# Kernel optimization log

Hardware: AMD Instinct MI355X
Metric: run time of the kernel (lower is better)

The kernel has to match this reference:

```python
import jax, jax.numpy as jnp
from jax import lax
import numpy as np

N_ATOMS, N_BONDS, N_GRAPHS = 8192, 32768, 256
EMBED, HIDDEN, DEPTH = 32, 256, 10
ATOM_VOCAB, BOND_VOCAB = 200, 10


def setup_inputs() -> dict:
    key = jax.random.key(0)
    ks = jax.random.split(key, 16)
    f = lambda k, *sh: jax.random.normal(k, sh, dtype=jnp.float32) * 0.05
    return {
        "atom_features": jax.random.randint(ks[0], (N_ATOMS,), 0, ATOM_VOCAB),
        "bond_features": jax.random.randint(ks[1], (N_BONDS,), 0, BOND_VOCAB),
        "adjacency_matrix": jax.random.randint(ks[2], (N_ATOMS, N_ATOMS), 0, 2, dtype=jnp.int32),
        "batch_indices": jax.random.randint(ks[3], (N_ATOMS,), 0, N_GRAPHS),
        "atom_emb": f(ks[4], ATOM_VOCAB, EMBED),
        "bond_emb": f(ks[5], BOND_VOCAB, EMBED),
        "msg_W": f(ks[6], DEPTH, HIDDEN, 2 * EMBED),
        "msg_b": f(ks[7], DEPTH, HIDDEN),
        "gru_Wih": f(ks[8], DEPTH, 3 * EMBED, HIDDEN),
        "gru_Whh": f(ks[9], DEPTH, 3 * EMBED, EMBED),
        "gru_bih": f(ks[10], DEPTH, 3 * EMBED),
        "gru_bhh": f(ks[11], DEPTH, 3 * EMBED),
        "pool_W": f(ks[12], HIDDEN, EMBED),
        "pool_b": f(ks[13], HIDDEN),
    }


def _gmpn(atom_emb, bond_emb, msg_W, msg_b, gru_Wih, gru_Whh, gru_bih, gru_bhh,
          pool_W, pool_b, atom_features, bond_features, adjacency_matrix, batch_indices):
    H = atom_emb[atom_features]                       # [N, E]
    A = (adjacency_matrix > 0).astype(H.dtype)        # [N, N] 0/1
    deg = A.sum(axis=1)                               # [N]
    has_nb = deg > 0
    inv_deg = jnp.where(has_nb, 1.0 / jnp.maximum(deg, 1.0), 0.0)[:, None]

    def layer(h, params):
        W, b, wih, whh, b_ih, b_hh = params
        # mean_j Linear([h_i ; h_j]) = W1 h_i + W2 mean_j h_j + b
        neigh_mean = (A @ h) * inv_deg                # [N, E]
        W1, W2 = W[:, :EMBED], W[:, EMBED:]
        msg = h @ W1.T + neigh_mean @ W2.T + b        # [N, HIDDEN]
        msg = jnp.where(has_nb[:, None], msg, 0.0)    # zero message if no neighbors
        # single-step GRU: input=msg, hidden state=h
        gi = msg @ wih.T + b_ih
        gh = h @ whh.T + b_hh
        ir, iz, inn = jnp.split(gi, 3, axis=-1)
        hr, hz, hn = jnp.split(gh, 3, axis=-1)
        r = jax.nn.sigmoid(ir + hr)
        z = jax.nn.sigmoid(iz + hz)
        n = jnp.tanh(inn + r * hn)
        h_new = (1.0 - z) * n + z * h                 # [N, E]
        return h_new, None

    H, _ = lax.scan(layer, H, (msg_W, msg_b, gru_Wih, gru_Whh, gru_bih, gru_bhh))

    # per-graph mean pooling (zeros for empty graphs), then global_pool linear
    seg_sum = jax.ops.segment_sum(H, batch_indices, num_segments=N_GRAPHS)
    cnt = jax.ops.segment_sum(jnp.ones((H.shape[0],), H.dtype), batch_indices, num_segments=N_GRAPHS)
    graph_mean = jnp.where(cnt[:, None] > 0, seg_sum / jnp.maximum(cnt, 1.0)[:, None], 0.0)
    graph_embeddings = graph_mean @ pool_W.T + pool_b  # [G, HIDDEN]

    bond_embeddings = bond_emb[bond_features]          # [B, E]
    return H, bond_embeddings, graph_embeddings


def reference(atom_features, bond_features, adjacency_matrix, batch_indices,
              atom_emb, bond_emb, msg_W, msg_b, gru_Wih, gru_Whh, gru_bih, gru_bhh,
              pool_W, pool_b):
    return _gmpn(atom_emb, bond_emb, msg_W, msg_b, gru_Wih, gru_Whh, gru_bih, gru_bhh,
                 pool_W, pool_b, atom_features, bond_features, adjacency_matrix, batch_indices)
```

## Files before the change

kernel.cpp:

```cpp
#include <hip/hip_runtime.h>
#include <stdint.h>

typedef __bf16 bf16x8 __attribute__((ext_vector_type(8)));
typedef float f32x4 __attribute__((ext_vector_type(4)));

__device__ __forceinline__ float b2f(unsigned short u){
  unsigned int t = ((unsigned int)u) << 16;
  return __builtin_bit_cast(float, t);
}
__device__ __forceinline__ unsigned short f2b(float f){
  unsigned int x = __builtin_bit_cast(unsigned int, f);
  x = x + 0x7FFFu + ((x >> 16) & 1u);
  return (unsigned short)(x >> 16);
}
__device__ __forceinline__ void spread8(unsigned int B, unsigned int w[4]){
  unsigned int m = __umul24(B, 0x8001u);
  w[0] = __umul24(m & 0x00010001u, 0x3F80u);
  w[1] = __umul24(m & 0x00040004u, 0x0FE0u);
  w[2] = __umul24(m & 0x00100010u, 0x03F8u);
  w[3] = __umul24(m & 0x00400040u, 0x00FEu);
}
__device__ __forceinline__ float fsig(float x){ return 1.f/(1.f + __expf(-x)); }
__device__ __forceinline__ float ftanh(float x){ return 1.f - 2.f/(__expf(2.f*x) + 1.f); }

__global__ void k_init(const int* __restrict__ adj, unsigned int* __restrict__ mask3,
                       int* __restrict__ deg,
                       const void* s_msgW, const void* s_msgb, const void* s_wih,
                       const void* s_whh, const void* s_bih, const void* s_bhh,
                       const void* s_poolW, const void* s_poolb,
                       const unsigned short* __restrict__ aemb_u16,
                       const int* __restrict__ bft, const void* __restrict__ braw,
                       unsigned short* __restrict__ cw,
                       float* __restrict__ seg, float* __restrict__ cnt,
                       int* __restrict__ flag,
                       unsigned short* __restrict__ outB16, float* __restrict__ outB32){
  int b = blockIdx.x, t = threadIdx.x;
  if (b < 8192){
    int tid = b*256 + t;
    int rb  = tid >> 12;
    int rem = tid & 4095;
    int kgg = rem >> 6;
    int L   = rem & 63;
    int lc = L & 15, q = L >> 4;
    int row = rb*16 + lc;
    const int* arow = adj + (size_t)row*8192 + kgg*128 + q*8;
    unsigned int dw = 0; int pc = 0;
    #pragma unroll
    for (int s=0;s<4;s++){
      const int* p = arow + s*32;
      unsigned int bb = 0;
      #pragma unroll
      for (int j=0;j<8;j++) bb |= (p[j] > 0 ? 1u : 0u) << j;
      dw |= bb << (8*s);
      pc += __popc(bb);
    }
    mask3[tid] = dw;
    pc += __shfl_xor(pc, 16);
    pc += __shfl_xor(pc, 32);
    if (q == 0) atomicAdd(deg + row, pc);
    return;
  }
  unsigned int uu = aemb_u16[2*t];
  int e = (int)((uu >> 7) & 0xFF);
  unsigned long long vote = __ballot(e >= 100 && e <= 127);
  int isb = (__popcll(vote) > 32) ? 1 : 0;
  if (b < 9963){
    int id = (b - 8192)*256 + t;
    if (id < 453248){
      const void* src; int off;
      if      (id < 163840){ src = s_msgW;  off = id; }
      else if (id < 166400){ src = s_msgb;  off = id - 163840; }
      else if (id < 412160){ src = s_wih;   off = id - 166400; }
      else if (id < 442880){ src = s_whh;   off = id - 412160; }
      else if (id < 443840){ src = s_bih;   off = id - 442880; }
      else if (id < 444800){ src = s_bhh;   off = id - 443840; }
      else if (id < 452992){ src = s_poolW; off = id - 444800; }
      else                 { src = s_poolb; off = id - 452992; }
      cw[id] = isb ? ((const unsigned short*)src)[off]
                   : f2b(((const float*)src)[off]);
    }
  } else if (b < 9996){
    int id2 = (b - 9963)*256 + t;
    if (id2 < 8192) seg[id2] = 0.f;
    if (id2 < 256) cnt[id2] = 0.f;
    if (b == 9963 && t == 0) flag[0] = isb;
  } else {
    int id = (b - 9996)*256 + t;
    int e2 = id >> 5, c = id & 31;
    int idx = bft[e2]*32 + c;
    if (isb) outB16[id] = ((const unsigned short*)braw)[idx];
    else     outB32[id] = ((const float*)braw)[idx];
  }
}

__global__ void k_zero(int* __restrict__ deg){
  deg[blockIdx.x*256 + threadIdx.x] = 0;
}

__global__ void k_embed(const int* __restrict__ af, const void* __restrict__ araw,
                        const int* __restrict__ flag,
                        float* __restrict__ hf32, uint4* __restrict__ hfrag){
  __shared__ __align__(16) float sh[512];
  int t = threadIdx.x;
  int r = t >> 5, c = t & 31;
  int row = blockIdx.x*16 + r;
  int idx = af[row]*32 + c;
  float f;
  if (flag[0]) f = b2f(((const unsigned short*)araw)[idx]);
  else         f = ((const float*)araw)[idx];
  hf32[row*32 + c] = f;
  sh[r*32 + c] = f;
  __syncthreads();
  if (t < 64){
    int nt = t >> 5, Lq = t & 31;
    int ks32 = blockIdx.x >> 1, half = blockIdx.x & 1;
    int col = nt*16 + (Lq & 15);
    int rbase = (Lq >> 4)*8;
    unsigned int w[4];
    #pragma unroll
    for (int p=0;p<4;p++){
      unsigned int lo = f2b(sh[(rbase + 2*p    )*32 + col]);
      unsigned int hi = f2b(sh[(rbase + 2*p + 1)*32 + col]);
      w[p] = lo | (hi << 16);
    }
    hfrag[(ks32*2 + nt)*64 + half*32 + Lq] = make_uint4(w[0],w[1],w[2],w[3]);
  }
}

__launch_bounds__(512, 1)
__global__ void k_layer(const unsigned int* __restrict__ mask3,
                        const uint4* __restrict__ hfragIn,
                        unsigned int* __restrict__ hfragOut,
                        float* __restrict__ hf32,
                        const int* __restrict__ deg,
                        const unsigned short* __restrict__ msgW,
                        const unsigned short* __restrict__ msgb,
                        const unsigned short* __restrict__ wih,
                        const unsigned short* __restrict__ whh,
                        const unsigned short* __restrict__ bih,
                        const unsigned short* __restrict__ bhh,
                        const int* __restrict__ bidx,
                        float* __restrict__ seg, float* __restrict__ cnt,
                        unsigned short* __restrict__ out16, float* __restrict__ out32,
                        const int* __restrict__ flag, int last)
{
  __shared__ __align__(16) float uni[8448];
  __shared__ __align__(16) unsigned short sA[32][72];
  __shared__ __align__(16) unsigned short smsg[32][264];
  __shared__ int sdeg[32];

  const int t = threadIdx.x, b = blockIdx.x;
  const int w = t >> 6, L = t & 63;
  const int q = L >> 4, lc = L & 15;
  const int r0 = t >> 4;
  const int cl = t & 15;
  const int r  = b*32 + r0;
  const int isb = flag[0];
  const int dgr = deg[r];
  const float invr = dgr > 0 ? 1.f/(float)dgr : 0.f;
  float h0 = hf32[r*32 + cl];
  float h1 = hf32[r*32 + 16 + cl];
  sA[r0][cl]    = f2b(h0);
  sA[r0][16+cl] = f2b(h1);
  if (cl == 0) sdeg[r0] = dgr;

  {
    f32x4 a00={0,0,0,0}, a01={0,0,0,0}, a10={0,0,0,0}, a11={0,0,0,0};
    const unsigned int* mp = mask3 + (size_t)b*8192 + w*512 + L;
    const uint4* bp = hfragIn + (size_t)w*4096 + L;
    unsigned int mw0 = mp[0];
    unsigned int mw1 = mp[4096];
    uint4 cb[8];
    #pragma unroll
    for (int s=0;s<4;s++){ cb[2*s] = bp[s*128]; cb[2*s+1] = bp[s*128 + 64]; }
    for (int g=0; g<8; g++){
      unsigned int nm0 = 0, nm1 = 0;
      uint4 nb[8];
      if (g < 7){
        nm0 = mp[(g+1)*64];
        nm1 = mp[4096 + (g+1)*64];
        #pragma unroll
        for (int s=0;s<4;s++){
          nb[2*s]   = bp[((g+1)*4 + s)*128];
          nb[2*s+1] = bp[((g+1)*4 + s)*128 + 64];
        }
      }
      #pragma unroll
      for (int s=0; s<4; s++){
        union { unsigned int u[4]; bf16x8 v; } A0, A1, B0, B1;
        spread8((mw0 >> (8*s)) & 0xFFu, A0.u);
        spread8((mw1 >> (8*s)) & 0xFFu, A1.u);
        uint4 u0 = cb[2*s], u1 = cb[2*s+1];
        B0.u[0]=u0.x; B0.u[1]=u0.y; B0.u[2]=u0.z; B0.u[3]=u0.w;
        B1.u[0]=u1.x; B1.u[1]=u1.y; B1.u[2]=u1.z; B1.u[3]=u1.w;
        a00 = __builtin_amdgcn_mfma_f32_16x16x32_bf16(A0.v, B0.v, a00, 0,0,0);
        a01 = __builtin_amdgcn_mfma_f32_16x16x32_bf16(A0.v, B1.v, a01, 0,0,0);
        a10 = __builtin_amdgcn_mfma_f32_16x16x32_bf16(A1.v, B0.v, a10, 0,0,0);
        a11 = __builtin_amdgcn_mfma_f32_16x16x32_bf16(A1.v, B1.v, a11, 0,0,0);
      }
      mw0 = nm0; mw1 = nm1;
      if (g < 7){
        #pragma unroll
        for (int u=0;u<8;u++) cb[u] = nb[u];
      }
    }
    float* sp = uni + w*1056;
    #pragma unroll
    for (int rg=0; rg<4; rg++){
      int rw = q*4 + rg;
      sp[rw*33 + lc]         = a00[rg];
      sp[rw*33 + 16 + lc]    = a01[rg];
      sp[(16+rw)*33 + lc]    = a10[rg];
      sp[(16+rw)*33 + 16+lc] = a11[rg];
    }
  }
  __syncthreads();
  {
    float s0 = 0.f, s1 = 0.f;
    #pragma unroll
    for (int ww=0; ww<8; ww++){
      s0 += uni[ww*1056 + r0*33 + cl];
      s1 += uni[ww*1056 + r0*33 + 16 + cl];
    }
    sA[r0][32+cl] = f2b(s0*invr);
    sA[r0][48+cl] = f2b(s1*invr);
  }
  __syncthreads();
  {
    int rt = w & 1, ntb = (w >> 1)*4;
    union { uint4 u; bf16x8 v; } A0, A1;
    A0.u = *(const uint4*)&sA[rt*16 + lc][q*8];
    A1.u = *(const uint4*)&sA[rt*16 + lc][32 + q*8];
    int sd[4];
    #pragma unroll
    for (int rg=0; rg<4; rg++) sd[rg] = sdeg[rt*16 + q*4 + rg];
    #pragma unroll
    for (int i=0; i<4; i++){
      int nt = ntb + i;
      union { uint4 u; bf16x8 v; } B0, B1;
      B0.u = *(const uint4*)(msgW + (size_t)(nt*16 + lc)*64 + q*8);
      B1.u = *(const uint4*)(msgW + (size_t)(nt*16 + lc)*64 + 32 + q*8);
      f32x4 am = {0,0,0,0};
      am = __builtin_amdgcn_mfma_f32_16x16x32_bf16(A0.v, B0.v, am, 0,0,0);
      am = __builtin_amdgcn_mfma_f32_16x16x32_bf16(A1.v, B1.v, am, 0,0,0);
      float bv = b2f(msgb[nt*16 + lc]);
      #pragma unroll
      for (int rg=0; rg<4; rg++){
        int rw = rt*16 + q*4 + rg;
        float v = am[rg] + bv;
        if (sd[rg] == 0) v = 0.f;
        smsg[rw][nt*16 + lc] = f2b(v);
      }
    }
  }
  __syncthreads();
  {
    float* sgi = uni;
    float* sgh = uni + 3200;
    if (w < 6){
      int nt = w;
      f32x4 g0 = {0,0,0,0}, g1 = {0,0,0,0};
      #pragma unroll
      for (int ks=0; ks<8; ks++){
        union { uint4 u; bf16x8 v; } A0, A1, B;
        B.u  = *(const uint4*)(wih + (size_t)(nt*16 + lc)*256 + ks*32 + q*8);
        A0.u = *(const uint4*)&smsg[lc][ks*32 + q*8];
        A1.u = *(const uint4*)&smsg[16 + lc][ks*32 + q*8];
        g0 = __builtin_amdgcn_mfma_f32_16x16x32_bf16(A0.v, B.v, g0, 0,0,0);
        g1 = __builtin_amdgcn_mfma_f32_16x16x32_bf16(A1.v, B.v, g1, 0,0,0);
      }
      #pragma unroll
      for (int rg=0; rg<4; rg++){
        sgi[(q*4+rg)*100    + nt*16 + lc] = g0[rg];
        sgi[(16+q*4+rg)*100 + nt*16 + lc] = g1[rg];
      }
    } else {
      int rt = w - 6;
      union { uint4 u; bf16x8 v; } A;
      A.u = *(const uint4*)&sA[rt*16 + lc][q*8];
      #pragma unroll
      for (int nt=0; nt<6; nt++){
        union { uint4 u; bf16x8 v; } B;
        B.u = *(const uint4*)(whh + (size_t)(nt*16 + lc)*32 + q*8);
        f32x4 hh = {0,0,0,0};
        hh = __builtin_amdgcn_mfma_f32_16x16x32_bf16(A.v, B.v, hh, 0,0,0);
        #pragma unroll
        for (int rg=0; rg<4; rg++)
          sgh[(rt*16 + q*4+rg)*100 + nt*16 + lc] = hh[rg];
      }
    }
  }
  __syncthreads();
  {
    const float* sgi = uni;
    const float* sgh = uni + 3200;
    float ir0 = sgi[r0*100 + cl]    + b2f(bih[cl]),    hr0 = sgh[r0*100 + cl]    + b2f(bhh[cl]);
    float iz0 = sgi[r0*100 + 32+cl] + b2f(bih[32+cl]), hz0 = sgh[r0*100 + 32+cl] + b2f(bhh[32+cl]);
    float in0 = sgi[r0*100 + 64+cl] + b2f(bih[64+cl]), hn0 = sgh[r0*100 + 64+cl] + b2f(bhh[64+cl]);
    float ir1 = sgi[r0*100 + 16+cl] + b2f(bih[16+cl]), hr1 = sgh[r0*100 + 16+cl] + b2f(bhh[16+cl]);
    float iz1 = sgi[r0*100 + 48+cl] + b2f(bih[48+cl]), hz1 = sgh[r0*100 + 48+cl] + b2f(bhh[48+cl]);
    float in1 = sgi[r0*100 + 80+cl] + b2f(bih[80+cl]), hn1 = sgh[r0*100 + 80+cl] + b2f(bhh[80+cl]);
    float rr0 = fsig(ir0 + hr0), zz0 = fsig(iz0 + hz0);
    float rr1 = fsig(ir1 + hr1), zz1 = fsig(iz1 + hz1);
    float nn0 = ftanh(in0 + rr0*hn0);
    float nn1 = ftanh(in1 + rr1*hn1);
    h0 = (1.f - zz0)*nn0 + zz0*h0;
    h1 = (1.f - zz1)*nn1 + zz1*h1;
    hf32[r*32 + cl]      = h0;
    hf32[r*32 + 16 + cl] = h1;
    unsigned int m0 = f2b(h0), m1 = f2b(h1);
    unsigned int p0 = (unsigned int)__shfl_xor((int)m0, 16);
    unsigned int p1 = (unsigned int)__shfl_xor((int)m1, 16);
    if ((r & 1) == 0){
      int ks32 = r >> 5, Lf = ((r >> 3) & 3)*16 + cl, pidx = (r & 7) >> 1;
      hfragOut[((ks32*2 + 0)*64 + Lf)*4 + pidx] = m0 | (p0 << 16);
      hfragOut[((ks32*2 + 1)*64 + Lf)*4 + pidx] = m1 | (p1 << 16);
    }
    if (last){
      if (isb){ out16[r*32 + cl] = (unsigned short)m0; out16[r*32 + 16 + cl] = (unsigned short)m1; }
      else    { out32[r*32 + cl] = h0; out32[r*32 + 16 + cl] = h1; }
      int gb = bidx[r];
      atomicAdd(seg + gb*32 + cl, h0);
      atomicAdd(seg + gb*32 + 16 + cl, h1);
      if (cl == 0) atomicAdd(cnt + gb, 1.f);
    }
  }
}

__global__ void k_pool(const float* __restrict__ seg, const float* __restrict__ cnt,
                       const unsigned short* __restrict__ pw, const unsigned short* __restrict__ pb,
                       const int* __restrict__ flag,
                       unsigned short* __restrict__ outG16, float* __restrict__ outG32){
  int g = blockIdx.x, o = threadIdx.x;
  float cv = cnt[g];
  float ic = cv > 0.f ? 1.f/cv : 0.f;
  float s = 0.f;
  #pragma unroll
  for (int c=0;c<32;c++) s += seg[g*32+c]*ic*b2f(pw[o*32+c]);
  s += b2f(pb[o]);
  if (flag[0]) outG16[g*256 + o] = f2b(s);
  else         outG32[g*256 + o] = s;
}

extern "C" void kernel_launch(void* const* d_in, const int* in_sizes, int n_in,
                              void* d_out, int out_size, void* d_ws, size_t ws_size,
                              hipStream_t stream){
  const int* af   = (const int*)d_in[0];
  const int* bft  = (const int*)d_in[1];
  const int* adj  = (const int*)d_in[2];
  const int* bidx = (const int*)d_in[3];

  char* ws = (char*)d_ws;
  unsigned int*   mask3  = (unsigned int*)(ws + 0);
  unsigned int*   hfrag0 = (unsigned int*)(ws + 8388608);
  unsigned int*   hfrag1 = (unsigned int*)(ws + 8912896);
  float*          hf32   = (float*)(ws + 9437184);
  int*            deg    = (int*)(ws + 10485760);
  float*          seg    = (float*)(ws + 10518528);
  float*          cnt    = (float*)(ws + 10551296);
  int*            flag   = (int*)(ws + 10552320);
  unsigned short* cw     = (unsigned short*)(ws + 10552384);

  unsigned short* o16 = (unsigned short*)d_out;
  float*          o32 = (float*)d_out;

  k_zero<<<32, 256, 0, stream>>>(deg);
  k_init<<<14092, 256, 0, stream>>>(adj, mask3, deg,
                                    d_in[6], d_in[7], d_in[8], d_in[9], d_in[10],
                                    d_in[11], d_in[12], d_in[13],
                                    (const unsigned short*)d_in[4],
                                    bft, d_in[5],
                                    cw, seg, cnt, flag,
                                    o16 + 262144, o32 + 262144);
  k_embed<<<512, 512, 0, stream>>>(af, d_in[4], flag, hf32, (uint4*)hfrag0);

  for (int d = 0; d < 10; d++){
    const uint4*  hin  = (const uint4*)((d & 1) ? hfrag1 : hfrag0);
    unsigned int* hout = (d & 1) ? hfrag0 : hfrag1;
    k_layer<<<256, 512, 0, stream>>>(mask3, hin, hout, hf32, deg,
                                     cw + (size_t)d*16384,          cw + 163840 + d*256,
                                     cw + 166400 + (size_t)d*24576, cw + 412160 + d*3072,
                                     cw + 442880 + d*96,            cw + 443840 + d*96,
                                     bidx, seg, cnt, o16, o32, flag, (d == 9) ? 1 : 0);
  }
  k_pool<<<256, 256, 0, stream>>>(seg, cnt, cw + 444800, cw + 452992, flag,
                                  o16 + 1310720, o32 + 1310720);
}
```

Before: 533.4 us.

## Double k_layer block to 1024 threads and drop register prefetch in A@h loop

Each 32-row block now runs 16 waves instead of 8. The adjacency-times-h reduction is split across 16 waves, each covering half as many K chunks, and the per-wave partial sums are combined through a larger shared buffer. The message, GRU input and GRU hidden matmuls are redistributed so each wave does fewer tiles, and the elementwise GRU uses one column per thread. The explicit software prefetch of the next mask/h-fragment chunk is removed, which relies on more waves in flight to hide latency. The trade-offs are more shared memory, a longer cross-wave reduction, and possible register pressure under the 1024-thread launch bound.

```diff
diff --git a/kernel.cpp b/kernel.cpp
--- a/kernel.cpp
+++ b/kernel.cpp
@@ -127,7 +127,7 @@
   }
 }
 
-__launch_bounds__(512, 1)
+__launch_bounds__(1024, 1)
 __global__ void k_layer(const unsigned int* __restrict__ mask3,
                         const uint4* __restrict__ hfragIn,
                         unsigned int* __restrict__ hfragOut,
@@ -144,7 +144,7 @@
                         unsigned short* __restrict__ out16, float* __restrict__ out32,
                         const int* __restrict__ flag, int last)
 {
-  __shared__ __align__(16) float uni[8448];
+  __shared__ __align__(16) float uni[16896];
   __shared__ __align__(16) unsigned short sA[32][72];
   __shared__ __align__(16) unsigned short smsg[32][264];
   __shared__ int sdeg[32];
@@ -152,45 +152,30 @@
   const int t = threadIdx.x, b = blockIdx.x;
   const int w = t >> 6, L = t & 63;
   const int q = L >> 4, lc = L & 15;
-  const int r0 = t >> 4;
-  const int cl = t & 15;
+  const int r0 = t >> 5;
+  const int c  = t & 31;
   const int r  = b*32 + r0;
   const int isb = flag[0];
   const int dgr = deg[r];
   const float invr = dgr > 0 ? 1.f/(float)dgr : 0.f;
-  float h0 = hf32[r*32 + cl];
-  float h1 = hf32[r*32 + 16 + cl];
-  sA[r0][cl]    = f2b(h0);
-  sA[r0][16+cl] = f2b(h1);
-  if (cl == 0) sdeg[r0] = dgr;
+  float h = hf32[r*32 + c];
+  sA[r0][c] = f2b(h);
+  if (c == 0) sdeg[r0] = dgr;
 
   {
     f32x4 a00={0,0,0,0}, a01={0,0,0,0}, a10={0,0,0,0}, a11={0,0,0,0};
-    const unsigned int* mp = mask3 + (size_t)b*8192 + w*512 + L;
-    const uint4* bp = hfragIn + (size_t)w*4096 + L;
-    unsigned int mw0 = mp[0];
-    unsigned int mw1 = mp[4096];
-    uint4 cb[8];
-    #pragma unroll
-    for (int s=0;s<4;s++){ cb[2*s] = bp[s*128]; cb[2*s+1] = bp[s*128 + 64]; }
-    for (int g=0; g<8; g++){
-      unsigned int nm0 = 0, nm1 = 0;
-      uint4 nb[8];
-      if (g < 7){
-        nm0 = mp[(g+1)*64];
-        nm1 = mp[4096 + (g+1)*64];
-        #pragma unroll
-        for (int s=0;s<4;s++){
-          nb[2*s]   = bp[((g+1)*4 + s)*128];
-          nb[2*s+1] = bp[((g+1)*4 + s)*128 + 64];
-        }
-      }
+    const unsigned int* mp = mask3 + (size_t)b*8192 + w*256 + L;
+    const uint4* bp = hfragIn + (size_t)w*2048 + L;
+    for (int g=0; g<4; g++){
+      unsigned int mw0 = mp[g*64];
+      unsigned int mw1 = mp[4096 + g*64];
       #pragma unroll
       for (int s=0; s<4; s++){
+        uint4 u0 = bp[(g*8 + s*2    )*64];
+        uint4 u1 = bp[(g*8 + s*2 + 1)*64];
         union { unsigned int u[4]; bf16x8 v; } A0, A1, B0, B1;
         spread8((mw0 >> (8*s)) & 0xFFu, A0.u);
         spread8((mw1 >> (8*s)) & 0xFFu, A1.u);
-        uint4 u0 = cb[2*s], u1 = cb[2*s+1];
         B0.u[0]=u0.x; B0.u[1]=u0.y; B0.u[2]=u0.z; B0.u[3]=u0.w;
         B1.u[0]=u1.x; B1.u[1]=u1.y; B1.u[2]=u1.z; B1.u[3]=u1.w;
         a00 = __builtin_amdgcn_mfma_f32_16x16x32_bf16(A0.v, B0.v, a00, 0,0,0);
@@ -198,11 +183,6 @@
         a10 = __builtin_amdgcn_mfma_f32_16x16x32_bf16(A1.v, B0.v, a10, 0,0,0);
         a11 = __builtin_amdgcn_mfma_f32_16x16x32_bf16(A1.v, B1.v, a11, 0,0,0);
       }
-      mw0 = nm0; mw1 = nm1;
-      if (g < 7){
-        #pragma unroll
-        for (int u=0;u<8;u++) cb[u] = nb[u];
-      }
     }
     float* sp = uni + w*1056;
     #pragma unroll
@@ -216,18 +196,14 @@
   }
   __syncthreads();
   {
-    float s0 = 0.f, s1 = 0.f;
-    #pragma unroll
-    for (int ww=0; ww<8; ww++){
-      s0 += uni[ww*1056 + r0*33 + cl];
-      s1 += uni[ww*1056 + r0*33 + 16 + cl];
-    }
-    sA[r0][32+cl] = f2b(s0*invr);
-    sA[r0][48+cl] = f2b(s1*invr);
-  }
-  __syncthreads();
-  {
-    int rt = w & 1, ntb = (w >> 1)*4;
+    float s = 0.f;
+    #pragma unroll
+    for (int ww=0; ww<16; ww++) s += uni[ww*1056 + r0*33 + c];
+    sA[r0][32 + c] = f2b(s*invr);
+  }
+  __syncthreads();
+  {
+    int rt = w & 1, ntb = (w >> 1)*2;
     union { uint4 u; bf16x8 v; } A0, A1;
     A0.u = *(const uint4*)&sA[rt*16 + lc][q*8];
     A1.u = *(const uint4*)&sA[rt*16 + lc][32 + q*8];
@@ -235,7 +211,7 @@
     #pragma unroll
     for (int rg=0; rg<4; rg++) sd[rg] = sdeg[rt*16 + q*4 + rg];
     #pragma unroll
-    for (int i=0; i<4; i++){
+    for (int i=0; i<2; i++){
       int nt = ntb + i;
       union { uint4 u; bf16x8 v; } B0, B1;
       B0.u = *(const uint4*)(msgW + (size_t)(nt*16 + lc)*64 + q*8);
@@ -257,29 +233,27 @@
   {
     float* sgi = uni;
     float* sgh = uni + 3200;
-    if (w < 6){
-      int nt = w;
-      f32x4 g0 = {0,0,0,0}, g1 = {0,0,0,0};
+    if (w < 12){
+      int nt = w >> 1, rt = w & 1;
+      f32x4 g0 = {0,0,0,0};
       #pragma unroll
       for (int ks=0; ks<8; ks++){
-        union { uint4 u; bf16x8 v; } A0, A1, B;
-        B.u  = *(const uint4*)(wih + (size_t)(nt*16 + lc)*256 + ks*32 + q*8);
-        A0.u = *(const uint4*)&smsg[lc][ks*32 + q*8];
-        A1.u = *(const uint4*)&smsg[16 + lc][ks*32 + q*8];
-        g0 = __builtin_amdgcn_mfma_f32_16x16x32_bf16(A0.v, B.v, g0, 0,0,0);
-        g1 = __builtin_amdgcn_mfma_f32_16x16x32_bf16(A1.v, B.v, g1, 0,0,0);
+        union { uint4 u; bf16x8 v; } A, B;
+        B.u = *(const uint4*)(wih + (size_t)(nt*16 + lc)*256 + ks*32 + q*8);
+        A.u = *(const uint4*)&smsg[rt*16 + lc][ks*32 + q*8];
+        g0 = __builtin_amdgcn_mfma_f32_16x16x32_bf16(A.v, B.v, g0, 0,0,0);
       }
       #pragma unroll
-      for (int rg=0; rg<4; rg++){
-        sgi[(q*4+rg)*100    + nt*16 + lc] = g0[rg];
-        sgi[(16+q*4+rg)*100 + nt*16 + lc] = g1[rg];
-      }
+      for (int rg=0; rg<4; rg++)
+        sgi[(rt*16 + q*4+rg)*100 + nt*16 + lc] = g0[rg];
     } else {
-      int rt = w - 6;
+      int idx = w - 12;
+      int rt = idx & 1, ntb = (idx >> 1)*3;
       union { uint4 u; bf16x8 v; } A;
       A.u = *(const uint4*)&sA[rt*16 + lc][q*8];
       #pragma unroll
-      for (int nt=0; nt<6; nt++){
+      for (int i=0; i<3; i++){
+        int nt = ntb + i;
         union { uint4 u; bf16x8 v; } B;
         B.u = *(const uint4*)(whh + (size_t)(nt*16 + lc)*32 + q*8);
         f32x4 hh = {0,0,0,0};
@@ -294,35 +268,27 @@
   {
     const float* sgi = uni;
     const float* sgh = uni + 3200;
-    float ir0 = sgi[r0*100 + cl]    + b2f(bih[cl]),    hr0 = sgh[r0*100 + cl]    + b2f(bhh[cl]);
-    float iz0 = sgi[r0*100 + 32+cl] + b2f(bih[32+cl]), hz0 = sgh[r0*100 + 32+cl] + b2f(bhh[32+cl]);
-    float in0 = sgi[r0*100 + 64+cl] + b2f(bih[64+cl]), hn0 = sgh[r0*100 + 64+cl] + b2f(bhh[64+cl]);
-    float ir1 = sgi[r0*100 + 16+cl] + b2f(bih[16+cl]), hr1 = sgh[r0*100 + 16+cl] + b2f(bhh[16+cl]);
-    float iz1 = sgi[r0*100 + 48+cl] + b2f(bih[48+cl]), hz1 = sgh[r0*100 + 48+cl] + b2f(bhh[48+cl]);
-    float in1 = sgi[r0*100 + 80+cl] + b2f(bih[80+cl]), hn1 = sgh[r0*100 + 80+cl] + b2f(bhh[80+cl]);
-    float rr0 = fsig(ir0 + hr0), zz0 = fsig(iz0 + hz0);
-    float rr1 = fsig(ir1 + hr1), zz1 = fsig(iz1 + hz1);
-    float nn0 = ftanh(in0 + rr0*hn0);
-    float nn1 = ftanh(in1 + rr1*hn1);
-    h0 = (1.f - zz0)*nn0 + zz0*h0;
-    h1 = (1.f - zz1)*nn1 + zz1*h1;
-    hf32[r*32 + cl]      = h0;
-    hf32[r*32 + 16 + cl] = h1;
-    unsigned int m0 = f2b(h0), m1 = f2b(h1);
-    unsigned int p0 = (unsigned int)__shfl_xor((int)m0, 16);
-    unsigned int p1 = (unsigned int)__shfl_xor((int)m1, 16);
+    float ir = sgi[r0*100 + c]    + b2f(bih[c]),    hr = sgh[r0*100 + c]    + b2f(bhh[c]);
+    float iz = sgi[r0*100 + 32+c] + b2f(bih[32+c]), hz = sgh[r0*100 + 32+c] + b2f(bhh[32+c]);
+    float in = sgi[r0*100 + 64+c] + b2f(bih[64+c]), hn = sgh[r0*100 + 64+c] + b2f(bhh[64+c]);
+    float rr = fsig(ir + hr), zz = fsig(iz + hz);
+    float nn = ftanh(in + rr*hn);
+    h = (1.f - zz)*nn + zz*h;
+    hf32[r*32 + c] = h;
+    unsigned int m = f2b(h);
+    unsigned int p = (unsigned int)__shfl_xor((int)m, 32);
     if ((r & 1) == 0){
-      int ks32 = r >> 5, Lf = ((r >> 3) & 3)*16 + cl, pidx = (r & 7) >> 1;
-      hfragOut[((ks32*2 + 0)*64 + Lf)*4 + pidx] = m0 | (p0 << 16);
-      hfragOut[((ks32*2 + 1)*64 + Lf)*4 + pidx] = m1 | (p1 << 16);
+      int ks32 = r >> 5, nt = c >> 4;
+      int Lf = ((r >> 3) & 3)*16 + (c & 15);
+      int pidx = (r & 7) >> 1;
+      hfragOut[((ks32*2 + nt)*64 + Lf)*4 + pidx] = m | (p << 16);
     }
     if (last){
-      if (isb){ out16[r*32 + cl] = (unsigned short)m0; out16[r*32 + 16 + cl] = (unsigned short)m1; }
-      else    { out32[r*32 + cl] = h0; out32[r*32 + 16 + cl] = h1; }
+      if (isb) out16[r*32 + c] = (unsigned short)m;
+      else     out32[r*32 + c] = h;
       int gb = bidx[r];
-      atomicAdd(seg + gb*32 + cl, h0);
-      atomicAdd(seg + gb*32 + 16 + cl, h1);
-      if (cl == 0) atomicAdd(cnt + gb, 1.f);
+      atomicAdd(seg + gb*32 + c, h);
+      if (c == 0) atomicAdd(cnt + gb, 1.f);
     }
   }
 }
@@ -377,11 +343,11 @@
   for (int d = 0; d < 10; d++){
     const uint4*  hin  = (const uint4*)((d & 1) ? hfrag1 : hfrag0);
     unsigned int* hout = (d & 1) ? hfrag0 : hfrag1;
-    k_layer<<<256, 512, 0, stream>>>(mask3, hin, hout, hf32, deg,
-                                     cw + (size_t)d*16384,          cw + 163840 + d*256,
-                                     cw + 166400 + (size_t)d*24576, cw + 412160 + d*3072,
-                                     cw + 442880 + d*96,            cw + 443840 + d*96,
-                                     bidx, seg, cnt, o16, o32, flag, (d == 9) ? 1 : 0);
+    k_layer<<<256, 1024, 0, stream>>>(mask3, hin, hout, hf32, deg,
+                                      cw + (size_t)d*16384,          cw + 163840 + d*256,
+                                      cw + 166400 + (size_t)d*24576, cw + 412160 + d*3072,
+                                      cw + 442880 + d*96,            cw + 443840 + d*96,
+                                      bidx, seg, cnt, o16, o32, flag, (d == 9) ? 1 : 0);
   }
   k_pool<<<256, 256, 0, stream>>>(seg, cnt, cw + 444800, cw + 452992, flag,
                                   o16 + 1310720, o32 + 1310720);
```

Measured after the change: 545.6 us. 2.3% more time.
